# Kernel optimization log

Hardware: AMD Instinct MI355X
Metric: run time of the kernel (lower is better)

The kernel has to match this reference:

```python
import jax, jax.numpy as jnp
import numpy as np

B, T, D = 4, 4096, 4096
G, C, K, M = 1, 4, 128, 32          # num_groups, n_splits, dw_hidden_dim, heads_per_group
I2 = 4                               # qkw inner dim = 2 * dynamic_hidden_dim (dyn_hidden = 32//16 = 2)
EPS = 1.1920929e-07                  # torch F.rms_norm default eps for fp32


def _rms_norm(x):
    # F.rms_norm over last dim, no learned scale
    return x * jax.lax.rsqrt(jnp.mean(x * x, axis=-1, keepdims=True) + EPS)


def setup_inputs() -> dict:
    key = jax.random.key(0)
    k0, k1, k2, k3 = jax.random.split(key, 4)
    dw1_std = np.sqrt(2.0 / (D + K))
    qkw_std = 0.02 / (np.sqrt(2 * 32 * 2) * (32 + 2))
    dd_std = 0.05 * np.sqrt(2.0 / (32 + D))
    return {
        "query_vec": jax.random.normal(k0, (B, T, D), dtype=jnp.float32),
        "dw1": jax.random.normal(k1, (D, G, C, K), dtype=jnp.float32) * dw1_std,
        "qkw": jax.random.normal(k2, (G, C, K, I2, M), dtype=jnp.float32) * qkw_std,
        "dd": jax.random.normal(k3, (D, G, M * C), dtype=jnp.float32) * dd_std,
        "norm_scale": jnp.ones((G,), dtype=jnp.float32) * 0.001,
    }


def reference(query_vec, dw1, qkw, dd, norm_scale):
    # dw_hidden: [B,T,G,C,K]
    dw_hidden = jnp.einsum('btd,dgck->btgck', query_vec, dw1)
    dw_hidden = jax.nn.gelu(dw_hidden, approximate=False)  # torch nn.GELU() is exact
    # w: [B,T,G,C,I2,M]
    w = jnp.einsum('btgck,gckim->btgcim', dw_hidden, qkw)
    half = qkw.shape[-2] // 2
    w1 = _rms_norm(w[..., :half, :])
    w2 = _rms_norm(w[..., half:, :]) * norm_scale  # norm_scale [G]=(1,) broadcasts over M
    # squeeze group dim (keep_group_dim=False) -> [B,T,C,I,M]
    w1 = w1[:, :, 0]
    w2 = w2[:, :, 0]
    # unbind along C: order pre_q, pre_k, post_q, post_k; key-wise pieces are discarded
    pre_qw1, post_qw1 = w1[:, :, 0], w1[:, :, 2]
    pre_qw2, post_qw2 = w2[:, :, 0], w2[:, :, 2]
    # dd: [B,T,G,M*C] -> tanh -> squeeze G -> split 4
    dd_out = jnp.tanh(jnp.einsum('btd,dgm->btgm', query_vec, dd))[:, :, 0]
    pre_qdd = dd_out[..., 0 * M:1 * M]
    post_qdd = dd_out[..., 2 * M:3 * M]
    # pack all live outputs into one array [B, T, 2*(2*I*M) + 2*M]
    flat = lambda a: a.reshape(a.shape[0], a.shape[1], -1)
    return jnp.concatenate(
        [flat(pre_qw1), flat(pre_qw2), pre_qdd,
         flat(post_qw1), flat(post_qw2), post_qdd], axis=-1)
```

## Files before the change

kernel.cpp:

```cpp
#include <hip/hip_runtime.h>
#include <cstdint>
#include <cstddef>

typedef __bf16 bf16x8 __attribute__((ext_vector_type(8)));
typedef float f32x4 __attribute__((ext_vector_type(4)));

#define D_DIM 4096
#define NCOL 320
#define BM 64
#define NKT 128
#define EPS_F 1.1920929e-07f
#define HS 136
#define ABYTES 8192
#define STG 28672
#define RING 4
#define SMEM (RING * STG)

__device__ __forceinline__ void gld16(const void* g, void* l) {
  __builtin_amdgcn_global_load_lds(
      (const __attribute__((address_space(1))) unsigned int*)g,
      (__attribute__((address_space(3))) unsigned int*)l,
      16, 0, 0);
}

__global__ void dwp_pack(const float* __restrict__ dw1,
                         const float* __restrict__ qkw,
                         const float* __restrict__ dd,
                         __bf16* __restrict__ Wp,
                         __bf16* __restrict__ Qt) {
  const int b = blockIdx.x;
  const int t = threadIdx.x;
  if (b < 128) {
    __shared__ __bf16 tile[10240];
    const int kt = b;
    const int kk = t >> 3;
    const int d = kt * 32 + kk;
    const int u = kk >> 3;
#pragma unroll
    for (int j = 0; j < 5; ++j) {
      const int n0 = ((t & 7) + j * 8) * 8;
      const float* src;
      if (n0 < 128)      src = dw1 + (size_t)d * 512 + n0;
      else if (n0 < 256) src = dw1 + (size_t)d * 512 + 128 + n0;
      else if (n0 < 288) src = dd + (size_t)d * 128 + (n0 - 256);
      else               src = dd + (size_t)d * 128 + (n0 - 224);
      f32x4 v0 = *(const f32x4*)src;
      f32x4 v1 = *(const f32x4*)(src + 4);
#pragma unroll
      for (int q = 0; q < 8; ++q) {
        const int n = n0 + q;
        const int pos = n * 32 + ((u ^ ((n >> 1) & 3)) << 3) + (kk & 7);
        tile[pos] = (__bf16)((q < 4) ? v0[q] : v1[q - 4]);
      }
    }
    __syncthreads();
    __bf16* dst = Wp + (size_t)kt * 10240;
#pragma unroll
    for (int k = 0; k < 5; ++k) {
      const int u16 = t + k * 256;
      *(bf16x8*)(dst + u16 * 8) = *(const bf16x8*)(tile + u16 * 8);
    }
  } else {
#pragma unroll
    for (int ii = 0; ii < 16; ++ii) {
      const int q = t + ii * 256;
      const int c2 = q >> 11;
      const int rem = q & 2047;
      const int n = rem >> 4;
      const int k0 = (rem & 15) * 8;
      const float* src = qkw + (size_t)c2 * 32768 + (size_t)k0 * 128 + n;
      bf16x8 v;
#pragma unroll
      for (int j = 0; j < 8; ++j) v[j] = (__bf16)src[(size_t)j * 128];
      *(bf16x8*)(Qt + (size_t)c2 * 16384 + (size_t)n * 128 + k0) = v;
    }
  }
}

__global__ __launch_bounds__(1024, 4) void dwp_main(
    const float* __restrict__ X,
    const __bf16* __restrict__ Wp,
    const __bf16* __restrict__ Qt,
    const float* __restrict__ NS,
    float* __restrict__ Out) {
  extern __shared__ __align__(16) unsigned char lds[];
  const int t = threadIdx.x;
  const int w = t >> 6;
  const int l = t & 63;
  const int lq = l >> 4;
  const int lm = l & 15;
  const int m0 = blockIdx.x * BM;

  const int rg = w >> 2;
  const int cg = w & 3;
  const int cbase = cg * 80;

  const int cnt = (w < 12) ? 2 : 1;
  const char* gsrc[2];
  int gstep[2];
  unsigned ldsoff[2];
#pragma unroll
  for (int i = 0; i < 2; ++i) {
    const int c = w + i * 16;
    if (i < cnt && c < 8) {
      const int row = c * 8 + (l >> 3);
      const int u = (l & 7) ^ (row & 7);
      gsrc[i] = (const char*)(X + (size_t)(m0 + row) * D_DIM) + u * 16;
      gstep[i] = 128;
      ldsoff[i] = (unsigned)(c * 1024);
    } else if (i < cnt) {
      const int cb = c - 8;
      gsrc[i] = (const char*)Wp + cb * 1024 + (size_t)l * 16;
      gstep[i] = 20480;
      ldsoff[i] = (unsigned)(ABYTES + cb * 1024);
    } else {
      gsrc[i] = nullptr; gstep[i] = 0; ldsoff[i] = 0;
    }
  }

  unsigned aoff0, aoff1, boff[5];
  {
    const int row = rg * 16 + lm;
    aoff0 = (unsigned)(row * 128 + (((lq * 2 + 0) ^ (lm & 7)) * 16));
    aoff1 = (unsigned)(row * 128 + (((lq * 2 + 1) ^ (lm & 7)) * 16));
  }
#pragma unroll
  for (int ct = 0; ct < 5; ++ct) {
    const int n = cbase + ct * 16 + lm;
    boff[ct] = (unsigned)(ABYTES + n * 64 + ((lq ^ ((n >> 1) & 3)) << 4));
  }

  f32x4 acc[5];
#pragma unroll
  for (int ct = 0; ct < 5; ++ct) acc[ct] = (f32x4){0.f, 0.f, 0.f, 0.f};

  auto issue = [&](int kt, int slot) {
    unsigned char* base = lds + slot * STG;
#pragma unroll
    for (int i = 0; i < 2; ++i)
      if (i < cnt)
        gld16(gsrc[i] + (size_t)kt * gstep[i], base + ldsoff[i]);
  };

  auto body = [&](int kt, int slot) {
    const unsigned char* cb = lds + slot * STG;
    bf16x8 a, b[5];
    f32x4 x0 = *(const f32x4*)(cb + aoff0);
    f32x4 x1 = *(const f32x4*)(cb + aoff1);
#pragma unroll
    for (int j = 0; j < 4; ++j) {
      a[j] = (__bf16)x0[j];
      a[4 + j] = (__bf16)x1[j];
    }
#pragma unroll
    for (int ct = 0; ct < 5; ++ct) b[ct] = *(const bf16x8*)(cb + boff[ct]);
#pragma unroll
    for (int ct = 0; ct < 5; ++ct)
      acc[ct] =
          __builtin_amdgcn_mfma_f32_16x16x32_bf16(a, b[ct], acc[ct], 0, 0, 0);
  };

  issue(0, 0);
  issue(1, 1);
  issue(2, 2);

  for (int kt = 0; kt < NKT - 3; ++kt) {
    if (w < 12) asm volatile("s_waitcnt vmcnt(4)" ::: "memory");
    else        asm volatile("s_waitcnt vmcnt(2)" ::: "memory");
    asm volatile("s_barrier" ::: "memory");
    issue(kt + 3, (kt + 3) & 3);
    body(kt, kt & 3);
  }
  if (w < 12) asm volatile("s_waitcnt vmcnt(4)" ::: "memory");
  else        asm volatile("s_waitcnt vmcnt(2)" ::: "memory");
  asm volatile("s_barrier" ::: "memory");
  body(NKT - 3, (NKT - 3) & 3);
  if (w < 12) asm volatile("s_waitcnt vmcnt(2)" ::: "memory");
  else        asm volatile("s_waitcnt vmcnt(1)" ::: "memory");
  asm volatile("s_barrier" ::: "memory");
  body(NKT - 2, (NKT - 2) & 3);
  asm volatile("s_waitcnt vmcnt(0)" ::: "memory");
  asm volatile("s_barrier" ::: "memory");
  body(NKT - 1, (NKT - 1) & 3);

  __syncthreads();

  const float ns = NS[0];

#pragma unroll
  for (int ct = 0; ct < 5; ++ct) {
    const int ncol = cbase + ct * 16 + lm;
    const int rowb = rg * 16 + lq * 4;
    f32x4 v = acc[ct];
    if (ncol < 256) {
      const int c2 = ncol >> 7;
      const int kcol = ncol & 127;
#pragma unroll
      for (int j = 0; j < 4; ++j) {
        float x = v[j];
        float g = 0.5f * x * (1.0f + erff(x * 0.70710678118f));
        *(__bf16*)(lds + (size_t)((c2 * 64 + rowb + j) * HS + kcol) * 2) = (__bf16)g;
      }
    } else {
      const int nd = ncol - 256;
      const int off = (nd < 32) ? (128 + nd) : (256 + nd);
#pragma unroll
      for (int j = 0; j < 4; ++j)
        Out[(size_t)(m0 + rowb + j) * NCOL + off] = tanhf(v[j]);
    }
  }
  __syncthreads();

  const int c2b = w >> 3;
  const int iq = (w >> 1) & 3;
  const int rh = w & 1;
  const int nnb = iq * 32;
  f32x4 acc2[2][2];
#pragma unroll
  for (int rt = 0; rt < 2; ++rt)
#pragma unroll
    for (int ct = 0; ct < 2; ++ct) acc2[rt][ct] = (f32x4){0.f, 0.f, 0.f, 0.f};

#pragma unroll
  for (int ks = 0; ks < 4; ++ks) {
    bf16x8 a2[2], b2[2];
#pragma unroll
    for (int rt = 0; rt < 2; ++rt)
      a2[rt] = *(const bf16x8*)(lds +
               (size_t)((c2b * 64 + rh * 32 + rt * 16 + lm) * HS + ks * 32 + lq * 8) * 2);
#pragma unroll
    for (int ct = 0; ct < 2; ++ct)
      b2[ct] = *(const bf16x8*)(Qt + (size_t)c2b * 16384 +
               (size_t)(nnb + ct * 16 + lm) * 128 + ks * 32 + lq * 8);
#pragma unroll
    for (int rt = 0; rt < 2; ++rt)
#pragma unroll
      for (int ct = 0; ct < 2; ++ct)
        acc2[rt][ct] =
            __builtin_amdgcn_mfma_f32_16x16x32_bf16(a2[rt], b2[ct], acc2[rt][ct], 0, 0, 0);
  }

  const float sce = (iq >= 2) ? ns : 1.0f;
#pragma unroll
  for (int rt = 0; rt < 2; ++rt) {
    f32x4 va = acc2[rt][0];
    f32x4 vb = acc2[rt][1];
#pragma unroll
    for (int j = 0; j < 4; ++j) {
      float s = va[j] * va[j] + vb[j] * vb[j];
      s += __shfl_xor(s, 1);
      s += __shfl_xor(s, 2);
      s += __shfl_xor(s, 4);
      s += __shfl_xor(s, 8);
      const float sc = rsqrtf(s * (1.0f / 32.0f) + EPS_F) * sce;
      const size_t row = (size_t)(m0 + rh * 32 + rt * 16 + lq * 4 + j);
      const int off = c2b * 160 + iq * 32;
      Out[row * NCOL + off + lm] = va[j] * sc;
      Out[row * NCOL + off + 16 + lm] = vb[j] * sc;
    }
  }
}

extern "C" void kernel_launch(void* const* d_in, const int* in_sizes, int n_in,
                              void* d_out, int out_size, void* d_ws, size_t ws_size,
                              hipStream_t stream) {
  const float* qv  = (const float*)d_in[0];
  const float* dw1 = (const float*)d_in[1];
  const float* qkw = (const float*)d_in[2];
  const float* dd  = (const float*)d_in[3];
  const float* ns  = (const float*)d_in[4];
  float* out = (float*)d_out;

  __bf16* Wp = (__bf16*)d_ws;
  __bf16* Qt = Wp + (size_t)4096 * 320;

  hipFuncSetAttribute((const void*)dwp_main,
                      hipFuncAttributeMaxDynamicSharedMemorySize, SMEM);

  dwp_pack<<<129, 256, 0, stream>>>(dw1, qkw, dd, Wp, Qt);
  dwp_main<<<256, 1024, SMEM, stream>>>(qv, Wp, Qt, ns, out);
}
```

Measured before the change: 426.0 us.

## Halve block to 512 threads with each wave computing two row tiles

Cuts the main kernel from 16 to 8 waves per block and gives each wave two 16-row tiles of A against five B column tiles. Each B fragment read from LDS now feeds two MFMAs. The load distribution, vmcnt wait counts and second-stage GEMM mapping are reworked to match. This lowers LDS read traffic per MFMA but doubles accumulator registers and leaves fewer waves to hide latency in the 256-block grid.

```diff
diff --git a/kernel.cpp b/kernel.cpp
--- a/kernel.cpp
+++ b/kernel.cpp
@@ -77,7 +77,7 @@
   }
 }
 
-__global__ __launch_bounds__(1024, 4) void dwp_main(
+__global__ __launch_bounds__(512, 2) void dwp_main(
     const float* __restrict__ X,
     const __bf16* __restrict__ Wp,
     const __bf16* __restrict__ Qt,
@@ -95,13 +95,13 @@
   const int cg = w & 3;
   const int cbase = cg * 80;
 
-  const int cnt = (w < 12) ? 2 : 1;
-  const char* gsrc[2];
-  int gstep[2];
-  unsigned ldsoff[2];
-#pragma unroll
-  for (int i = 0; i < 2; ++i) {
-    const int c = w + i * 16;
+  const int cnt = (w < 4) ? 4 : 3;
+  const char* gsrc[4];
+  int gstep[4];
+  unsigned ldsoff[4];
+#pragma unroll
+  for (int i = 0; i < 4; ++i) {
+    const int c = w + i * 8;
     if (i < cnt && c < 8) {
       const int row = c * 8 + (l >> 3);
       const int u = (l & 7) ^ (row & 7);
@@ -118,11 +118,12 @@
     }
   }
 
-  unsigned aoff0, aoff1, boff[5];
-  {
-    const int row = rg * 16 + lm;
-    aoff0 = (unsigned)(row * 128 + (((lq * 2 + 0) ^ (lm & 7)) * 16));
-    aoff1 = (unsigned)(row * 128 + (((lq * 2 + 1) ^ (lm & 7)) * 16));
+  unsigned aoff0[2], aoff1[2], boff[5];
+#pragma unroll
+  for (int rt = 0; rt < 2; ++rt) {
+    const int row = rg * 32 + rt * 16 + lm;
+    aoff0[rt] = (unsigned)(row * 128 + (((lq * 2 + 0) ^ (lm & 7)) * 16));
+    aoff1[rt] = (unsigned)(row * 128 + (((lq * 2 + 1) ^ (lm & 7)) * 16));
   }
 #pragma unroll
   for (int ct = 0; ct < 5; ++ct) {
@@ -130,34 +131,42 @@
     boff[ct] = (unsigned)(ABYTES + n * 64 + ((lq ^ ((n >> 1) & 3)) << 4));
   }
 
-  f32x4 acc[5];
-#pragma unroll
-  for (int ct = 0; ct < 5; ++ct) acc[ct] = (f32x4){0.f, 0.f, 0.f, 0.f};
+  f32x4 acc[2][5];
+#pragma unroll
+  for (int rt = 0; rt < 2; ++rt)
+#pragma unroll
+    for (int ct = 0; ct < 5; ++ct)
+      acc[rt][ct] = (f32x4){0.f, 0.f, 0.f, 0.f};
 
   auto issue = [&](int kt, int slot) {
     unsigned char* base = lds + slot * STG;
 #pragma unroll
-    for (int i = 0; i < 2; ++i)
+    for (int i = 0; i < 4; ++i)
       if (i < cnt)
         gld16(gsrc[i] + (size_t)kt * gstep[i], base + ldsoff[i]);
   };
 
   auto body = [&](int kt, int slot) {
     const unsigned char* cb = lds + slot * STG;
-    bf16x8 a, b[5];
-    f32x4 x0 = *(const f32x4*)(cb + aoff0);
-    f32x4 x1 = *(const f32x4*)(cb + aoff1);
-#pragma unroll
-    for (int j = 0; j < 4; ++j) {
-      a[j] = (__bf16)x0[j];
-      a[4 + j] = (__bf16)x1[j];
+    bf16x8 a[2], b[5];
+#pragma unroll
+    for (int rt = 0; rt < 2; ++rt) {
+      f32x4 x0 = *(const f32x4*)(cb + aoff0[rt]);
+      f32x4 x1 = *(const f32x4*)(cb + aoff1[rt]);
+#pragma unroll
+      for (int j = 0; j < 4; ++j) {
+        a[rt][j] = (__bf16)x0[j];
+        a[rt][4 + j] = (__bf16)x1[j];
+      }
     }
 #pragma unroll
     for (int ct = 0; ct < 5; ++ct) b[ct] = *(const bf16x8*)(cb + boff[ct]);
 #pragma unroll
-    for (int ct = 0; ct < 5; ++ct)
-      acc[ct] =
-          __builtin_amdgcn_mfma_f32_16x16x32_bf16(a, b[ct], acc[ct], 0, 0, 0);
+    for (int rt = 0; rt < 2; ++rt)
+#pragma unroll
+      for (int ct = 0; ct < 5; ++ct)
+        acc[rt][ct] =
+            __builtin_amdgcn_mfma_f32_16x16x32_bf16(a[rt], b[ct], acc[rt][ct], 0, 0, 0);
   };
 
   issue(0, 0);
@@ -165,18 +174,18 @@
   issue(2, 2);
 
   for (int kt = 0; kt < NKT - 3; ++kt) {
-    if (w < 12) asm volatile("s_waitcnt vmcnt(4)" ::: "memory");
-    else        asm volatile("s_waitcnt vmcnt(2)" ::: "memory");
+    if (w < 4) asm volatile("s_waitcnt vmcnt(8)" ::: "memory");
+    else       asm volatile("s_waitcnt vmcnt(6)" ::: "memory");
     asm volatile("s_barrier" ::: "memory");
     issue(kt + 3, (kt + 3) & 3);
     body(kt, kt & 3);
   }
-  if (w < 12) asm volatile("s_waitcnt vmcnt(4)" ::: "memory");
-  else        asm volatile("s_waitcnt vmcnt(2)" ::: "memory");
+  if (w < 4) asm volatile("s_waitcnt vmcnt(8)" ::: "memory");
+  else       asm volatile("s_waitcnt vmcnt(6)" ::: "memory");
   asm volatile("s_barrier" ::: "memory");
   body(NKT - 3, (NKT - 3) & 3);
-  if (w < 12) asm volatile("s_waitcnt vmcnt(2)" ::: "memory");
-  else        asm volatile("s_waitcnt vmcnt(1)" ::: "memory");
+  if (w < 4) asm volatile("s_waitcnt vmcnt(4)" ::: "memory");
+  else       asm volatile("s_waitcnt vmcnt(3)" ::: "memory");
   asm volatile("s_barrier" ::: "memory");
   body(NKT - 2, (NKT - 2) & 3);
   asm volatile("s_waitcnt vmcnt(0)" ::: "memory");
@@ -188,52 +197,54 @@
   const float ns = NS[0];
 
 #pragma unroll
-  for (int ct = 0; ct < 5; ++ct) {
-    const int ncol = cbase + ct * 16 + lm;
-    const int rowb = rg * 16 + lq * 4;
-    f32x4 v = acc[ct];
-    if (ncol < 256) {
-      const int c2 = ncol >> 7;
-      const int kcol = ncol & 127;
-#pragma unroll
-      for (int j = 0; j < 4; ++j) {
-        float x = v[j];
-        float g = 0.5f * x * (1.0f + erff(x * 0.70710678118f));
-        *(__bf16*)(lds + (size_t)((c2 * 64 + rowb + j) * HS + kcol) * 2) = (__bf16)g;
+  for (int rt = 0; rt < 2; ++rt) {
+#pragma unroll
+    for (int ct = 0; ct < 5; ++ct) {
+      const int ncol = cbase + ct * 16 + lm;
+      const int rowb = rg * 32 + rt * 16 + lq * 4;
+      f32x4 v = acc[rt][ct];
+      if (ncol < 256) {
+        const int c2 = ncol >> 7;
+        const int kcol = ncol & 127;
+#pragma unroll
+        for (int j = 0; j < 4; ++j) {
+          float x = v[j];
+          float g = 0.5f * x * (1.0f + erff(x * 0.70710678118f));
+          *(__bf16*)(lds + (size_t)((c2 * 64 + rowb + j) * HS + kcol) * 2) = (__bf16)g;
+        }
+      } else {
+        const int nd = ncol - 256;
+        const int off = (nd < 32) ? (128 + nd) : (256 + nd);
+#pragma unroll
+        for (int j = 0; j < 4; ++j)
+          Out[(size_t)(m0 + rowb + j) * NCOL + off] = tanhf(v[j]);
       }
-    } else {
-      const int nd = ncol - 256;
-      const int off = (nd < 32) ? (128 + nd) : (256 + nd);
-#pragma unroll
-      for (int j = 0; j < 4; ++j)
-        Out[(size_t)(m0 + rowb + j) * NCOL + off] = tanhf(v[j]);
     }
   }
   __syncthreads();
 
-  const int c2b = w >> 3;
-  const int iq = (w >> 1) & 3;
-  const int rh = w & 1;
+  const int c2b = w >> 2;
+  const int iq = w & 3;
   const int nnb = iq * 32;
-  f32x4 acc2[2][2];
-#pragma unroll
-  for (int rt = 0; rt < 2; ++rt)
+  f32x4 acc2[4][2];
+#pragma unroll
+  for (int rt = 0; rt < 4; ++rt)
 #pragma unroll
     for (int ct = 0; ct < 2; ++ct) acc2[rt][ct] = (f32x4){0.f, 0.f, 0.f, 0.f};
 
 #pragma unroll
   for (int ks = 0; ks < 4; ++ks) {
-    bf16x8 a2[2], b2[2];
-#pragma unroll
-    for (int rt = 0; rt < 2; ++rt)
+    bf16x8 a2[4], b2[2];
+#pragma unroll
+    for (int rt = 0; rt < 4; ++rt)
       a2[rt] = *(const bf16x8*)(lds +
-               (size_t)((c2b * 64 + rh * 32 + rt * 16 + lm) * HS + ks * 32 + lq * 8) * 2);
+               (size_t)((c2b * 64 + rt * 16 + lm) * HS + ks * 32 + lq * 8) * 2);
 #pragma unroll
     for (int ct = 0; ct < 2; ++ct)
       b2[ct] = *(const bf16x8*)(Qt + (size_t)c2b * 16384 +
                (size_t)(nnb + ct * 16 + lm) * 128 + ks * 32 + lq * 8);
 #pragma unroll
-    for (int rt = 0; rt < 2; ++rt)
+    for (int rt = 0; rt < 4; ++rt)
 #pragma unroll
       for (int ct = 0; ct < 2; ++ct)
         acc2[rt][ct] =
@@ -242,7 +253,7 @@
 
   const float sce = (iq >= 2) ? ns : 1.0f;
 #pragma unroll
-  for (int rt = 0; rt < 2; ++rt) {
+  for (int rt = 0; rt < 4; ++rt) {
     f32x4 va = acc2[rt][0];
     f32x4 vb = acc2[rt][1];
 #pragma unroll
@@ -253,7 +264,7 @@
       s += __shfl_xor(s, 4);
       s += __shfl_xor(s, 8);
       const float sc = rsqrtf(s * (1.0f / 32.0f) + EPS_F) * sce;
-      const size_t row = (size_t)(m0 + rh * 32 + rt * 16 + lq * 4 + j);
+      const size_t row = (size_t)(m0 + rt * 16 + lq * 4 + j);
       const int off = c2b * 160 + iq * 32;
       Out[row * NCOL + off + lm] = va[j] * sc;
       Out[row * NCOL + off + 16 + lm] = vb[j] * sc;
@@ -278,5 +289,5 @@
                       hipFuncAttributeMaxDynamicSharedMemorySize, SMEM);
 
   dwp_pack<<<129, 256, 0, stream>>>(dw1, qkw, dd, Wp, Qt);
-  dwp_main<<<256, 1024, SMEM, stream>>>(qv, Wp, Qt, ns, out);
-}
+  dwp_main<<<256, 512, SMEM, stream>>>(qv, Wp, Qt, ns, out);
+}
```

Measured after the change: 427.0 us. About the same (+0.2%).
